# Kernel tuning notes

Measured on AMD Instinct MI355X. Metric: run time of the kernel, lower is better.

Reference implementation:

```python
import jax, jax.numpy as jnp
import numpy as np

F_DIM, P_DIM, H_DIM, N_EXP = 768, 512, 1024, 4
B, T = 8192, 8192


def _gelu(x):
    return jax.nn.gelu(x, approximate=False)


def _normalize(x, eps=1e-12):
    n = jnp.linalg.norm(x, axis=-1, keepdims=True)
    return x / jnp.maximum(n, eps)


def setup_inputs() -> dict:
    key = jax.random.key(0)
    ks = jax.random.split(key, 24)
    s = 0.02
    inp = {
        'image_features': jax.random.normal(ks[0], (B, F_DIM), jnp.float32),
        'text_features': jax.random.normal(ks[1], (B, F_DIM), jnp.float32),
        'target_features': jax.random.normal(ks[2], (T, F_DIM), jnp.float32),
        # projection layers (torch Linear convention: W [out,in])
        'Wt': jax.random.normal(ks[3], (P_DIM, F_DIM), jnp.float32) * s,
        'bt': jnp.zeros((P_DIM,), jnp.float32),
        'Wi': jax.random.normal(ks[4], (P_DIM, F_DIM), jnp.float32) * s,
        'bi': jnp.zeros((P_DIM,), jnp.float32),
        # dynamic scalar MLP: (2P -> H -> 1)
        'ds_W1': jax.random.normal(ks[5], (H_DIM, 2 * P_DIM), jnp.float32) * s,
        'ds_b1': jnp.zeros((H_DIM,), jnp.float32),
        'ds_W2': jax.random.normal(ks[6], (1, H_DIM), jnp.float32) * s,
        'ds_b2': jnp.zeros((1,), jnp.float32),
        # experts stacked: [E, H, 2P]
        'exp_W': jax.random.normal(ks[7], (N_EXP, H_DIM, 2 * P_DIM), jnp.float32) * s,
        'exp_b': jnp.zeros((N_EXP, H_DIM), jnp.float32),
        # router: (2P -> H/4 -> E)
        'rt_W1': jax.random.normal(ks[8], (H_DIM // 4, 2 * P_DIM), jnp.float32) * s,
        'rt_b1': jnp.zeros((H_DIM // 4,), jnp.float32),
        'rt_W2': jax.random.normal(ks[9], (N_EXP, H_DIM // 4), jnp.float32) * s,
        'rt_b2': jnp.zeros((N_EXP,), jnp.float32),
        # output layer: (H -> F)
        'out_W': jax.random.normal(ks[10], (F_DIM, H_DIM), jnp.float32) * s,
        'out_b': jnp.zeros((F_DIM,), jnp.float32),
        'logit_scale': jnp.asarray(np.log(50.0), jnp.float32),
    }
    return inp


def reference(image_features, text_features, target_features, Wt, bt, Wi, bi,
              ds_W1, ds_b1, ds_W2, ds_b2, exp_W, exp_b,
              rt_W1, rt_b1, rt_W2, rt_b2, out_W, out_b, logit_scale):
    # eval mode: all dropouts are identity, no modality drop
    tp = _gelu(text_features @ Wt.T + bt)            # [B,P]
    ip = _gelu(image_features @ Wi.T + bi)           # [B,P]
    comb = jnp.concatenate([tp, ip], axis=-1)        # [B,2P]

    router_logits = _gelu(comb @ rt_W1.T + rt_b1) @ rt_W2.T + rt_b2  # [B,E]
    router_probs = jax.nn.softmax(router_logits, axis=-1)

    expert_out = _gelu(jnp.einsum('bd,ehd->beh', comb, exp_W) + exp_b)  # [B,E,H]
    fused_hidden = jnp.einsum('be,beh->bh', router_probs, expert_out)   # [B,H]
    residual = fused_hidden @ out_W.T + out_b                            # [B,F]

    ds = jax.nn.sigmoid(_gelu(comb @ ds_W1.T + ds_b1) @ ds_W2.T + ds_b2)  # [B,1]
    output = ds * text_features + (1.0 - ds) * image_features + residual
    pred = _normalize(output)
    tgt = _normalize(target_features)
    logits = jnp.exp(logit_scale) * (pred @ tgt.T)   # [B,T]
    return (logits, ds, router_probs)
```

## Files before the change

kernel.cpp:

```cpp
#include <hip/hip_runtime.h>
#include <stdint.h>
#include <math.h>

#define BDIM 8192
#define TDIM 8192
#define FDIM 768
#define PDIM 512
#define HDIM 1024
#define NEXP 4
#define NCAT 5376

using short4v = __attribute__((ext_vector_type(4))) short;
using short8 = __attribute__((ext_vector_type(8))) short;
using f32x4  = __attribute__((ext_vector_type(4))) float;

__device__ __forceinline__ short f2bf(float f) {
  uint32_t u = __builtin_bit_cast(uint32_t, f);
  u += 0x7fffu + ((u >> 16) & 1u);
  return (short)(u >> 16);
}
__device__ __forceinline__ float bf2f(short s) {
  uint32_t u = ((uint32_t)(uint16_t)s) << 16;
  return __builtin_bit_cast(float, u);
}
__device__ __forceinline__ float gelu_exact(float x) {
  return 0.5f * x * (1.0f + erff(x * 0.70710678118654752f));
}

#define GLDS(gp, lp) __builtin_amdgcn_global_load_lds( \
    (const __attribute__((address_space(1))) void*)(gp), \
    (__attribute__((address_space(3))) void*)(lp), 16, 0, 0)

template <int MODE>
__global__ __launch_bounds__(512, 2)
void gemm256(const short* __restrict__ A, int lda,
             const short* __restrict__ B, int ldb,
             void* __restrict__ C, int ldc, int K,
             const float* __restrict__ bias,
             const float* __restrict__ scale_ptr)
{
  __shared__ short lds_s[65536];
  const int t    = threadIdx.x;
  const int lane = t & 63;
  const int wave = t >> 6;
  const int wr   = wave >> 2;
  const int wc   = wave & 3;
  const int l15  = lane & 15;
  const int quad = lane >> 4;
  const int m0 = blockIdx.y * 256;
  const int n0 = blockIdx.x * 256;
  const int NT = K >> 5;

  float scale = 1.f;
  if (MODE == 2) scale = expf(scale_ptr[0]);

  const uint32_t Sl   = (uint32_t)t * 16u;
  const uint32_t Ssw  = Sl ^ (((Sl >> 7) & 7u) << 4);
  const uint32_t srow = Ssw >> 6;
  const uint32_t sk   = ((Ssw >> 4) & 3u) * 8u;
  const short* gA0 = A + (size_t)(m0 + srow) * lda + sk;
  const short* gA1 = A + (size_t)(m0 + 128 + srow) * lda + sk;
  const short* gB0 = B + (size_t)(n0 + srow) * ldb + sk;
  const short* gB1 = B + (size_t)(n0 + 128 + srow) * ldb + sk;
  short* lp = lds_s + t * 8;

#define STAGE_A(kt) { const int tb = ((kt) & 3) << 14; const int kk = (kt) << 5; \
    GLDS(gA0 + kk, lp + tb); GLDS(gA1 + kk, lp + tb + 4096); }
#define STAGE_B(kt) { const int tb = ((kt) & 3) << 14; const int kk = (kt) << 5; \
    GLDS(gB0 + kk, lp + tb + 8192); GLDS(gB1 + kk, lp + tb + 12288); }

  int offA[8], offB[4];
#pragma unroll
  for (int x = 0; x < 8; ++x) {
    uint32_t S = (uint32_t)((wr * 128 + (x >> 2) * 64 + (x & 3) * 16 + l15) * 64 + quad * 16);
    offA[x] = (int)((S ^ (((S >> 7) & 7u) << 4)) >> 1);
  }
#pragma unroll
  for (int j = 0; j < 4; ++j) {
    uint32_t S = (uint32_t)((wc * 64 + j * 16 + l15) * 64 + quad * 16);
    offB[j] = (int)(((S ^ (((S >> 7) & 7u) << 4)) >> 1) + 8192u);
  }

  f32x4 acc[8][4];
#pragma unroll
  for (int i = 0; i < 8; ++i)
#pragma unroll
    for (int j = 0; j < 4; ++j)
      acc[i][j] = (f32x4){0.f, 0.f, 0.f, 0.f};

  STAGE_A(0); STAGE_B(0);
  if (NT > 1) { STAGE_A(1); STAGE_B(1); }
  if (NT > 2) { STAGE_A(2); STAGE_B(2); }
  if (NT > 2)      asm volatile("s_waitcnt vmcnt(8)" ::: "memory");
  else if (NT > 1) asm volatile("s_waitcnt vmcnt(4)" ::: "memory");
  else             asm volatile("s_waitcnt vmcnt(0)" ::: "memory");
  asm volatile("s_barrier" ::: "memory");

  for (int kt = 0; kt < NT; ++kt) {
    const short* tile = lds_s + ((kt & 3) << 14);
    short8 a[4], b[4];
    if (kt + 3 < NT) { STAGE_A(kt + 3); }
#pragma unroll
    for (int j = 0; j < 4; ++j) b[j] = *(const short8*)(tile + offB[j]);
#pragma unroll
    for (int i = 0; i < 4; ++i) a[i] = *(const short8*)(tile + offA[i]);
    __builtin_amdgcn_s_setprio(1);
#pragma unroll
    for (int i = 0; i < 4; ++i)
#pragma unroll
      for (int j = 0; j < 4; ++j)
        acc[i][j] = __builtin_amdgcn_mfma_f32_16x16x32_bf16(a[i], b[j], acc[i][j], 0, 0, 0);
    __builtin_amdgcn_s_setprio(0);
    asm volatile("s_barrier" ::: "memory");
    if (kt + 3 < NT) { STAGE_B(kt + 3); }
#pragma unroll
    for (int i = 0; i < 4; ++i) a[i] = *(const short8*)(tile + offA[4 + i]);
    __builtin_amdgcn_s_setprio(1);
#pragma unroll
    for (int i = 0; i < 4; ++i)
#pragma unroll
      for (int j = 0; j < 4; ++j)
        acc[4 + i][j] = __builtin_amdgcn_mfma_f32_16x16x32_bf16(a[i], b[j], acc[4 + i][j], 0, 0, 0);
    __builtin_amdgcn_s_setprio(0);
    if (kt < NT - 1) {
      if (kt + 3 < NT)      asm volatile("s_waitcnt vmcnt(8) lgkmcnt(0)" ::: "memory");
      else if (kt + 2 < NT) asm volatile("s_waitcnt vmcnt(4) lgkmcnt(0)" ::: "memory");
      else                  asm volatile("s_waitcnt vmcnt(0) lgkmcnt(0)" ::: "memory");
      asm volatile("s_barrier" ::: "memory");
    }
  }
#undef STAGE_A
#undef STAGE_B

#pragma unroll
  for (int mh = 0; mh < 2; ++mh) {
#pragma unroll
    for (int i = 0; i < 4; ++i) {
      const int rowb = m0 + wr * 128 + mh * 64 + i * 16 + quad * 4;
#pragma unroll
      for (int j = 0; j < 4; ++j) {
        const int col = n0 + wc * 64 + j * 16 + l15;
        const float bv = (MODE == 2) ? 0.f : bias[col];
        f32x4 v = acc[mh * 4 + i][j];
#pragma unroll
        for (int r = 0; r < 4; ++r) {
          float x = v[r];
          if (MODE == 0) {
            ((short*)C)[(size_t)(rowb + r) * ldc + col] = f2bf(gelu_exact(x + bv));
          } else if (MODE == 1) {
            ((float*)C)[(size_t)(rowb + r) * ldc + col] = x + bv;
          } else {
            ((float*)C)[(size_t)(rowb + r) * ldc + col] = x * scale;
          }
        }
      }
    }
  }
}

template <int MODE>
__device__ __forceinline__ void gemm_body(
    const short* __restrict__ A, int lda,
    const short* __restrict__ B, int ldb,
    void* __restrict__ C, int ldc, int K,
    const float* __restrict__ bias, float scale,
    int m0, int n0)
{
  __shared__ short sA[4096];
  __shared__ short sB[4096];
  const int t    = threadIdx.x;
  const int lane = t & 63;
  const int wave = t >> 6;
  const int wm = (wave >> 1) * 64;
  const int wn = (wave & 1) * 64;
  const int l15  = lane & 15;
  const int quad = lane >> 4;

  f32x4 acc[4][4];
#pragma unroll
  for (int i = 0; i < 4; ++i)
#pragma unroll
    for (int j = 0; j < 4; ++j)
      acc[i][j] = (f32x4){0.f, 0.f, 0.f, 0.f};

  const int rr = t >> 2;
  const int cc = (t & 3) * 8;
  const short* gA0 = A + (size_t)(m0 + rr) * lda + cc;
  const short* gA1 = A + (size_t)(m0 + 64 + rr) * lda + cc;
  const short* gB0 = B + (size_t)(n0 + rr) * ldb + cc;
  const short* gB1 = B + (size_t)(n0 + 64 + rr) * ldb + cc;
  short* lA0 = sA + t * 8;
  short* lA1 = sA + 2048 + t * 8;
  short* lB0 = sB + t * 8;
  short* lB1 = sB + 2048 + t * 8;

  for (int k0 = 0; k0 < K; k0 += 32) {
    GLDS(gA0 + k0, lA0);
    GLDS(gA1 + k0, lA1);
    GLDS(gB0 + k0, lB0);
    GLDS(gB1 + k0, lB1);
    __syncthreads();
    short8 af[4], bfr[4];
#pragma unroll
    for (int i = 0; i < 4; ++i)
      af[i] = *(const short8*)(sA + (wm + i * 16 + l15) * 32 + quad * 8);
#pragma unroll
    for (int j = 0; j < 4; ++j)
      bfr[j] = *(const short8*)(sB + (wn + j * 16 + l15) * 32 + quad * 8);
#pragma unroll
    for (int i = 0; i < 4; ++i)
#pragma unroll
      for (int j = 0; j < 4; ++j)
        acc[i][j] = __builtin_amdgcn_mfma_f32_16x16x32_bf16(af[i], bfr[j], acc[i][j], 0, 0, 0);
    __syncthreads();
  }

#pragma unroll
  for (int i = 0; i < 4; ++i) {
#pragma unroll
    for (int j = 0; j < 4; ++j) {
      const int col = n0 + wn + j * 16 + l15;
      float bv = (MODE == 2) ? 0.f : bias[col];
#pragma unroll
      for (int r = 0; r < 4; ++r) {
        const int row = m0 + wm + i * 16 + quad * 4 + r;
        float v = acc[i][j][r];
        if (MODE == 0) {
          v = gelu_exact(v + bv);
          ((short*)C)[(size_t)row * ldc + col] = f2bf(v);
        } else if (MODE == 1) {
          ((float*)C)[(size_t)row * ldc + col] = v + bv;
        } else {
          ((float*)C)[(size_t)row * ldc + col] = v * scale;
        }
      }
    }
  }
}

template <int MODE>
__global__ __launch_bounds__(256, 2)
void gemm_bt(const short* __restrict__ A, int lda,
             const short* __restrict__ B, int ldb,
             void* __restrict__ C, int ldc, int K,
             const float* __restrict__ bias,
             const float* __restrict__ scale_ptr)
{
  float scale = 1.f;
  if (MODE == 2) scale = expf(scale_ptr[0]);
  gemm_body<MODE>(A, lda, B, ldb, C, ldc, K, bias, scale,
                  blockIdx.y * 128, blockIdx.x * 128);
}

__global__ __launch_bounds__(256, 2)
void gemm_proj(const short* __restrict__ textb, const short* __restrict__ imgb,
               const short* __restrict__ Wtb, const short* __restrict__ Wib,
               const float* __restrict__ bt, const float* __restrict__ bi,
               short* __restrict__ comb)
{
  const int z = blockIdx.z;
  const short* A = z ? imgb : textb;
  const short* B = z ? Wib : Wtb;
  const float* bias = z ? bi : bt;
  short* C = comb + (z ? 512 : 0);
  gemm_body<0>(A, FDIM, B, FDIM, C, 1024, FDIM, bias, 1.f,
               blockIdx.y * 128, blockIdx.x * 128);
}

#define SEG0 1572864u
#define SEG1 3145728u
#define SEG2 3244032u
#define SEG3 3342336u
#define SEG4 4390912u
#define SEG5 4653056u
#define SEG6 4718592u
#define SEG7 4915200u
#define SEG8 4916544u

__global__ __launch_bounds__(256)
void prep_all(const float* __restrict__ text, const float* __restrict__ image,
              const float* __restrict__ Wt, const float* __restrict__ Wi,
              const float* __restrict__ exp_W, const float* __restrict__ ds_W1,
              const float* __restrict__ rt_W1, const float* __restrict__ out_W,
              const float* __restrict__ exp_b, const float* __restrict__ ds_b1,
              const float* __restrict__ rt_b1,
              short* __restrict__ textb, short* __restrict__ imgb,
              short* __restrict__ Wtb, short* __restrict__ Wib,
              short* __restrict__ Bcat, short* __restrict__ outWb,
              float* __restrict__ biascat)
{
  const uint32_t i = blockIdx.x * 256 + threadIdx.x;
  if (i >= SEG8) return;
  if (i >= SEG7) {
    const uint32_t j = (i - SEG7) * 4;
#pragma unroll
    for (int k = 0; k < 4; ++k) {
      uint32_t idx = j + k;
      float v;
      if (idx < 4096)      v = exp_b[idx];
      else if (idx < 5120) v = ds_b1[idx - 4096];
      else                 v = rt_b1[idx - 5120];
      biascat[idx] = v;
    }
    return;
  }
  const float* s;
  short* d;
  uint32_t j;
  if (i < SEG1) {
    if (i < SEG0) { j = i;        s = text;  d = textb; }
    else          { j = i - SEG0; s = image; d = imgb;  }
  } else if (i < SEG3) {
    if (i < SEG2) { j = i - SEG1; s = Wt; d = Wtb; }
    else          { j = i - SEG2; s = Wi; d = Wib; }
  } else if (i < SEG5) {
    if (i < SEG4) { j = i - SEG3; s = exp_W; d = Bcat; }
    else          { j = i - SEG4; s = ds_W1; d = Bcat + (size_t)4096 * 1024; }
  } else {
    if (i < SEG6) { j = i - SEG5; s = rt_W1; d = Bcat + (size_t)5120 * 1024; }
    else          { j = i - SEG6; s = out_W; d = outWb; }
  }
  float4 v = ((const float4*)s)[j];
  short4v o = { f2bf(v.x), f2bf(v.y), f2bf(v.z), f2bf(v.w) };
  ((short4v*)d)[j] = o;
}

__global__ __launch_bounds__(256)
void moe_mix(const short* __restrict__ Hall,
             const float* __restrict__ rt_W2, const float* __restrict__ rt_b2,
             const float* __restrict__ ds_W2, const float* __restrict__ ds_b2,
             float* __restrict__ out_probs, float* __restrict__ out_ds,
             short* __restrict__ fused)
{
  const int b = blockIdx.x;
  const int t = threadIdx.x;
  const int lane = t & 63;
  const int wave = t >> 6;
  const short* h = Hall + (size_t)b * NCAT;

  float rv = bf2f(h[5120 + t]);
  float p0 = rv * rt_W2[t];
  float p1 = rv * rt_W2[256 + t];
  float p2 = rv * rt_W2[512 + t];
  float p3 = rv * rt_W2[768 + t];
  float dd = 0.f;
#pragma unroll
  for (int k = 0; k < 4; ++k)
    dd += bf2f(h[4096 + k * 256 + t]) * ds_W2[k * 256 + t];

#pragma unroll
  for (int off = 32; off; off >>= 1) {
    p0 += __shfl_xor(p0, off);
    p1 += __shfl_xor(p1, off);
    p2 += __shfl_xor(p2, off);
    p3 += __shfl_xor(p3, off);
    dd += __shfl_xor(dd, off);
  }
  __shared__ float red[5][4];
  __shared__ float bc[5];
  if (lane == 0) {
    red[0][wave] = p0; red[1][wave] = p1; red[2][wave] = p2;
    red[3][wave] = p3; red[4][wave] = dd;
  }
  __syncthreads();
  if (t == 0) {
    float l0 = red[0][0] + red[0][1] + red[0][2] + red[0][3] + rt_b2[0];
    float l1 = red[1][0] + red[1][1] + red[1][2] + red[1][3] + rt_b2[1];
    float l2 = red[2][0] + red[2][1] + red[2][2] + red[2][3] + rt_b2[2];
    float l3 = red[3][0] + red[3][1] + red[3][2] + red[3][3] + rt_b2[3];
    float d  = red[4][0] + red[4][1] + red[4][2] + red[4][3] + ds_b2[0];
    float mx = fmaxf(fmaxf(l0, l1), fmaxf(l2, l3));
    float e0 = expf(l0 - mx), e1 = expf(l1 - mx);
    float e2 = expf(l2 - mx), e3 = expf(l3 - mx);
    float inv = 1.f / (e0 + e1 + e2 + e3);
    bc[0] = e0 * inv; bc[1] = e1 * inv; bc[2] = e2 * inv; bc[3] = e3 * inv;
    bc[4] = 1.f / (1.f + expf(-d));
    out_probs[b * 4 + 0] = bc[0];
    out_probs[b * 4 + 1] = bc[1];
    out_probs[b * 4 + 2] = bc[2];
    out_probs[b * 4 + 3] = bc[3];
    out_ds[b] = bc[4];
  }
  __syncthreads();
  const float q0 = bc[0], q1 = bc[1], q2 = bc[2], q3 = bc[3];
  short* fr = fused + (size_t)b * 1024;
#pragma unroll
  for (int c = t; c < 1024; c += 256) {
    float v = q0 * bf2f(h[c])        + q1 * bf2f(h[1024 + c])
            + q2 * bf2f(h[2048 + c]) + q3 * bf2f(h[3072 + c]);
    fr[c] = f2bf(v);
  }
}

__global__ __launch_bounds__(256)
void normalize_both(const float* __restrict__ text, const float* __restrict__ image,
                    const float* __restrict__ ds, const float* __restrict__ resid,
                    const float* __restrict__ target,
                    short* __restrict__ pred, short* __restrict__ tgtb)
{
  const int bb = blockIdx.x;
  const int t = threadIdx.x;
  float o0, o1, o2;
  short* d;
  if (bb < BDIM) {
    const float dv = ds[bb];
    const float* tx = text + (size_t)bb * FDIM;
    const float* im = image + (size_t)bb * FDIM;
    const float* s  = resid + (size_t)bb * FDIM;
    o0 = dv * tx[t]       + (1.f - dv) * im[t]       + s[t];
    o1 = dv * tx[t + 256] + (1.f - dv) * im[t + 256] + s[t + 256];
    o2 = dv * tx[t + 512] + (1.f - dv) * im[t + 512] + s[t + 512];
    d = pred + (size_t)bb * FDIM;
  } else {
    const int b = bb - BDIM;
    const float* s = target + (size_t)b * FDIM;
    o0 = s[t]; o1 = s[t + 256]; o2 = s[t + 512];
    d = tgtb + (size_t)b * FDIM;
  }
  float ss = o0 * o0 + o1 * o1 + o2 * o2;
  __shared__ float red[4];
#pragma unroll
  for (int off = 32; off; off >>= 1) ss += __shfl_xor(ss, off);
  if ((t & 63) == 0) red[t >> 6] = ss;
  __syncthreads();
  const float tot = red[0] + red[1] + red[2] + red[3];
  const float rn = 1.f / fmaxf(sqrtf(tot), 1e-12f);
  d[t]       = f2bf(o0 * rn);
  d[t + 256] = f2bf(o1 * rn);
  d[t + 512] = f2bf(o2 * rn);
}

extern "C" void kernel_launch(void* const* d_in, const int* in_sizes, int n_in,
                              void* d_out, int out_size, void* d_ws, size_t ws_size,
                              hipStream_t stream) {
  const float* image  = (const float*)d_in[0];
  const float* text   = (const float*)d_in[1];
  const float* target = (const float*)d_in[2];
  const float* Wt     = (const float*)d_in[3];
  const float* bt     = (const float*)d_in[4];
  const float* Wi     = (const float*)d_in[5];
  const float* bi     = (const float*)d_in[6];
  const float* ds_W1  = (const float*)d_in[7];
  const float* ds_b1  = (const float*)d_in[8];
  const float* ds_W2  = (const float*)d_in[9];
  const float* ds_b2  = (const float*)d_in[10];
  const float* exp_W  = (const float*)d_in[11];
  const float* exp_b  = (const float*)d_in[12];
  const float* rt_W1  = (const float*)d_in[13];
  const float* rt_b1  = (const float*)d_in[14];
  const float* rt_W2  = (const float*)d_in[15];
  const float* rt_b2  = (const float*)d_in[16];
  const float* out_W  = (const float*)d_in[17];
  const float* out_b  = (const float*)d_in[18];
  const float* logit_scale = (const float*)d_in[19];

  char* ws = (char*)d_ws;
  short* comb  = (short*)ws;  ws += (size_t)BDIM * 1024 * 2;
  short* Hall  = (short*)ws;  ws += (size_t)BDIM * NCAT * 2;
  short* fused = (short*)ws;  ws += (size_t)BDIM * 1024 * 2;
  float* resid = (float*)ws;  ws += (size_t)BDIM * FDIM * 4;
  short* pred  = (short*)ws;  ws += (size_t)BDIM * FDIM * 2;
  short* tgtb  = (short*)ws;  ws += (size_t)TDIM * FDIM * 2;
  short* textb = (short*)ws;  ws += (size_t)BDIM * FDIM * 2;
  short* imgb  = (short*)ws;  ws += (size_t)BDIM * FDIM * 2;
  short* Wtb   = (short*)ws;  ws += (size_t)PDIM * FDIM * 2;
  short* Wib   = (short*)ws;  ws += (size_t)PDIM * FDIM * 2;
  short* outWb = (short*)ws;  ws += (size_t)FDIM * HDIM * 2;
  short* Bcat  = (short*)ws;  ws += (size_t)NCAT * HDIM * 2;
  float* biascat = (float*)ws; ws += (size_t)NCAT * 4;

  float* out_logits = (float*)d_out;
  float* out_ds     = out_logits + (size_t)BDIM * TDIM;
  float* out_probs  = out_ds + BDIM;

  prep_all<<<(SEG8 + 255) / 256, 256, 0, stream>>>(
      text, image, Wt, Wi, exp_W, ds_W1, rt_W1, out_W,
      exp_b, ds_b1, rt_b1,
      textb, imgb, Wtb, Wib, Bcat, outWb, biascat);

  dim3 blk(256);
  gemm_proj<<<dim3(PDIM / 128, BDIM / 128, 2), blk, 0, stream>>>(
      textb, imgb, Wtb, Wib, bt, bi, comb);
  gemm256<0><<<dim3(NCAT / 256, BDIM / 256), dim3(512), 0, stream>>>(
      comb, 1024, Bcat, 1024, Hall, NCAT, 1024, biascat, nullptr);
  moe_mix<<<BDIM, 256, 0, stream>>>(Hall, rt_W2, rt_b2, ds_W2, ds_b2,
                                    out_probs, out_ds, fused);
  gemm_bt<1><<<dim3(FDIM / 128, BDIM / 128), blk, 0, stream>>>(
      fused, 1024, outWb, 1024, resid, FDIM, 1024, out_b, nullptr);
  normalize_both<<<BDIM + TDIM, 256, 0, stream>>>(
      text, image, out_ds, resid, target, pred, tgtb);
  gemm256<2><<<dim3(TDIM / 256, BDIM / 256), dim3(512), 0, stream>>>(
      pred, FDIM, tgtb, FDIM, out_logits, TDIM, FDIM, nullptr, logit_scale);
}
```

Baseline: 673.4 us.

## Rework GEMM prefetch schedule with finer-grained staged loads and barriers

Restructures the 256x256 bf16 MFMA GEMM main loop: the wave-to-row mapping now interleaves row halves (mh*128 + wr*64), and the global-to-LDS prefetch is split into finer pieces, with tile T+2's three remaining quarters and tile T+3's first A quarter issued across the two compute phases. Extra s_barrier plus lgkmcnt(0) and sched_barrier points pin the LDS reads before each MFMA block. The aim is to spread memory traffic more evenly over compute and cut stalls. In exchange it adds barriers and more complex vmcnt accounting.

```diff
diff --git a/kernel.cpp b/kernel.cpp
--- a/kernel.cpp
+++ b/kernel.cpp
@@ -51,97 +51,117 @@
   const int n0 = blockIdx.x * 256;
   const int NT = K >> 5;
 
-  float scale = 1.f;
-  if (MODE == 2) scale = expf(scale_ptr[0]);
-
   const uint32_t Sl   = (uint32_t)t * 16u;
   const uint32_t Ssw  = Sl ^ (((Sl >> 7) & 7u) << 4);
   const uint32_t srow = Ssw >> 6;
   const uint32_t sk   = ((Ssw >> 4) & 3u) * 8u;
-  const short* gA0 = A + (size_t)(m0 + srow) * lda + sk;
-  const short* gA1 = A + (size_t)(m0 + 128 + srow) * lda + sk;
-  const short* gB0 = B + (size_t)(n0 + srow) * ldb + sk;
-  const short* gB1 = B + (size_t)(n0 + 128 + srow) * ldb + sk;
+  const short* gA    = A + (size_t)(m0 + srow) * lda + sk;
+  const short* gA128 = A + (size_t)(m0 + 128 + srow) * lda + sk;
+  const short* gB    = B + (size_t)(n0 + srow) * ldb + sk;
+  const short* gB128 = B + (size_t)(n0 + 128 + srow) * ldb + sk;
   short* lp = lds_s + t * 8;
 
-#define STAGE_A(kt) { const int tb = ((kt) & 3) << 14; const int kk = (kt) << 5; \
-    GLDS(gA0 + kk, lp + tb); GLDS(gA1 + kk, lp + tb + 4096); }
-#define STAGE_B(kt) { const int tb = ((kt) & 3) << 14; const int kk = (kt) << 5; \
-    GLDS(gB0 + kk, lp + tb + 8192); GLDS(gB1 + kk, lp + tb + 12288); }
-
-  int offA[8], offB[4];
-#pragma unroll
-  for (int x = 0; x < 8; ++x) {
-    uint32_t S = (uint32_t)((wr * 128 + (x >> 2) * 64 + (x & 3) * 16 + l15) * 64 + quad * 16);
-    offA[x] = (int)((S ^ (((S >> 7) & 7u) << 4)) >> 1);
+  int offA0[4], offB[4];
+#pragma unroll
+  for (int i = 0; i < 4; ++i) {
+    uint32_t S = (uint32_t)((wr * 64 + i * 16 + l15) * 64 + quad * 16);
+    offA0[i] = (int)((S ^ (((S >> 7) & 7u) << 4)) >> 1);
   }
 #pragma unroll
   for (int j = 0; j < 4; ++j) {
-    uint32_t S = (uint32_t)((wc * 64 + j * 16 + l15) * 64 + quad * 16);
-    offB[j] = (int)(((S ^ (((S >> 7) & 7u) << 4)) >> 1) + 8192u);
-  }
-
-  f32x4 acc[8][4];
-#pragma unroll
-  for (int i = 0; i < 8; ++i)
-#pragma unroll
-    for (int j = 0; j < 4; ++j)
-      acc[i][j] = (f32x4){0.f, 0.f, 0.f, 0.f};
-
-  STAGE_A(0); STAGE_B(0);
-  if (NT > 1) { STAGE_A(1); STAGE_B(1); }
-  if (NT > 2) { STAGE_A(2); STAGE_B(2); }
-  if (NT > 2)      asm volatile("s_waitcnt vmcnt(8)" ::: "memory");
-  else if (NT > 1) asm volatile("s_waitcnt vmcnt(4)" ::: "memory");
-  else             asm volatile("s_waitcnt vmcnt(0)" ::: "memory");
-  asm volatile("s_barrier" ::: "memory");
-
-  for (int kt = 0; kt < NT; ++kt) {
-    const short* tile = lds_s + ((kt & 3) << 14);
+    const int c = wc * 64 + j * 16 + l15;
+    uint32_t S = (uint32_t)((c & 127) * 64 + quad * 16);
+    offB[j] = (int)(((S ^ (((S >> 7) & 7u) << 4)) >> 1) + 8192u + (uint32_t)(c >> 7) * 4096u);
+  }
+
+  f32x4 acc[2][4][4];
+#pragma unroll
+  for (int h = 0; h < 2; ++h)
+#pragma unroll
+    for (int i = 0; i < 4; ++i)
+#pragma unroll
+      for (int j = 0; j < 4; ++j)
+        acc[h][i][j] = (f32x4){0.f, 0.f, 0.f, 0.f};
+
+  GLDS(gA,        lp +  0 * 4096);
+  GLDS(gA128,     lp +  1 * 4096);
+  GLDS(gB,        lp +  2 * 4096);
+  GLDS(gB128,     lp +  3 * 4096);
+  GLDS(gA + 32,   lp +  4 * 4096);
+  GLDS(gA128 + 32, lp + 5 * 4096);
+  GLDS(gB + 32,   lp +  6 * 4096);
+  GLDS(gB128 + 32, lp + 7 * 4096);
+  GLDS(gA + 64,   lp +  8 * 4096);
+  asm volatile("s_waitcnt vmcnt(5)" ::: "memory");
+  __builtin_amdgcn_s_barrier();
+
+  for (int T = 0; T < NT; ++T) {
+    const short* tile = lds_s + ((T & 3) << 14);
+    const int k2 = (T + 2) << 5;
+    const int k3 = (T + 3) << 5;
     short8 a[4], b[4];
-    if (kt + 3 < NT) { STAGE_A(kt + 3); }
+
+    if (T + 2 < NT) {
+      const int s2 = ((T + 2) & 3) << 14;
+      GLDS(gA128 + k2, lp + s2 + 4096);
+      GLDS(gB    + k2, lp + s2 + 8192);
+    }
 #pragma unroll
     for (int j = 0; j < 4; ++j) b[j] = *(const short8*)(tile + offB[j]);
 #pragma unroll
-    for (int i = 0; i < 4; ++i) a[i] = *(const short8*)(tile + offA[i]);
+    for (int i = 0; i < 4; ++i) a[i] = *(const short8*)(tile + offA0[i]);
+    __builtin_amdgcn_s_barrier();
+    asm volatile("s_waitcnt lgkmcnt(0)" ::: "memory");
+    __builtin_amdgcn_sched_barrier(0);
     __builtin_amdgcn_s_setprio(1);
 #pragma unroll
     for (int i = 0; i < 4; ++i)
 #pragma unroll
       for (int j = 0; j < 4; ++j)
-        acc[i][j] = __builtin_amdgcn_mfma_f32_16x16x32_bf16(a[i], b[j], acc[i][j], 0, 0, 0);
+        acc[0][i][j] = __builtin_amdgcn_mfma_f32_16x16x32_bf16(a[i], b[j], acc[0][i][j], 0, 0, 0);
     __builtin_amdgcn_s_setprio(0);
-    asm volatile("s_barrier" ::: "memory");
-    if (kt + 3 < NT) { STAGE_B(kt + 3); }
-#pragma unroll
-    for (int i = 0; i < 4; ++i) a[i] = *(const short8*)(tile + offA[4 + i]);
+    __builtin_amdgcn_s_barrier();
+
+    if (T + 2 < NT) {
+      const int s2 = ((T + 2) & 3) << 14;
+      GLDS(gB128 + k2, lp + s2 + 12288);
+    }
+    if (T + 3 < NT) {
+      const int s3 = ((T + 3) & 3) << 14;
+      GLDS(gA + k3, lp + s3);
+    }
+#pragma unroll
+    for (int i = 0; i < 4; ++i) a[i] = *(const short8*)(tile + offA0[i] + 4096);
+    __builtin_amdgcn_s_barrier();
+    asm volatile("s_waitcnt lgkmcnt(0)" ::: "memory");
+    __builtin_amdgcn_sched_barrier(0);
     __builtin_amdgcn_s_setprio(1);
 #pragma unroll
     for (int i = 0; i < 4; ++i)
 #pragma unroll
       for (int j = 0; j < 4; ++j)
-        acc[4 + i][j] = __builtin_amdgcn_mfma_f32_16x16x32_bf16(a[i], b[j], acc[4 + i][j], 0, 0, 0);
+        acc[1][i][j] = __builtin_amdgcn_mfma_f32_16x16x32_bf16(a[i], b[j], acc[1][i][j], 0, 0, 0);
     __builtin_amdgcn_s_setprio(0);
-    if (kt < NT - 1) {
-      if (kt + 3 < NT)      asm volatile("s_waitcnt vmcnt(8) lgkmcnt(0)" ::: "memory");
-      else if (kt + 2 < NT) asm volatile("s_waitcnt vmcnt(4) lgkmcnt(0)" ::: "memory");
-      else                  asm volatile("s_waitcnt vmcnt(0) lgkmcnt(0)" ::: "memory");
-      asm volatile("s_barrier" ::: "memory");
-    }
-  }
-#undef STAGE_A
-#undef STAGE_B
-
+    if (T < NT - 1) {
+      if      (T < NT - 3)  asm volatile("s_waitcnt vmcnt(5)" ::: "memory");
+      else if (T == NT - 3) asm volatile("s_waitcnt vmcnt(4)" ::: "memory");
+      else                  asm volatile("s_waitcnt vmcnt(0)" ::: "memory");
+      __builtin_amdgcn_s_barrier();
+    }
+  }
+
+  float scale = 1.f;
+  if (MODE == 2) scale = expf(scale_ptr[0]);
 #pragma unroll
   for (int mh = 0; mh < 2; ++mh) {
 #pragma unroll
     for (int i = 0; i < 4; ++i) {
-      const int rowb = m0 + wr * 128 + mh * 64 + i * 16 + quad * 4;
+      const int rowb = m0 + mh * 128 + wr * 64 + i * 16 + quad * 4;
 #pragma unroll
       for (int j = 0; j < 4; ++j) {
         const int col = n0 + wc * 64 + j * 16 + l15;
         const float bv = (MODE == 2) ? 0.f : bias[col];
-        f32x4 v = acc[mh * 4 + i][j];
+        f32x4 v = acc[mh][i][j];
 #pragma unroll
         for (int r = 0; r < 4; ++r) {
           float x = v[r];
```

After: 805.9 us. 19.7% more time.
